# Kernel optimization log

Hardware: AMD Instinct MI355X
Metric: run time of the kernel (lower is better)

## Reference

```python
import jax, jax.numpy as jnp
import numpy as np

SEQ, D_IN, D_OUT = 4096, 1024, 1024


def setup_inputs() -> dict:
    key = jax.random.key(0)
    k_emb, k_q, k_k, k_v = jax.random.split(key, 4)
    # torch Linear stores weight as [out, in]; we keep [in, out] for x @ W
    scale = 1.0 / np.sqrt(D_IN)
    return {
        "embeddings": jax.random.normal(k_emb, (SEQ, D_IN), dtype=jnp.float32),
        "w_query": jax.random.uniform(k_q, (D_IN, D_OUT), dtype=jnp.float32, minval=-scale, maxval=scale),
        "w_key": jax.random.uniform(k_k, (D_IN, D_OUT), dtype=jnp.float32, minval=-scale, maxval=scale),
        "w_value": jax.random.uniform(k_v, (D_IN, D_OUT), dtype=jnp.float32, minval=-scale, maxval=scale),
    }


def reference(embeddings, w_query, w_key, w_value):
    # QKV projections (bias=False)
    q = embeddings @ w_query  # [S, D_out]
    k = embeddings @ w_key    # [S, D_out]
    v = embeddings @ w_value  # [S, D_out]
    inv_sqrt_d = 1.0 / jnp.sqrt(jnp.asarray(k.shape[-1], dtype=q.dtype))
    scores = jnp.einsum("sd,td->st", q, k) * inv_sqrt_d  # [S, S]
    weights = jax.nn.softmax(scores, axis=-1)
    return weights @ v  # [S, D_out]
```

## Files before the change

kernel.cpp:

```cpp
#include <hip/hip_runtime.h>
#include <hip/hip_bf16.h>

typedef unsigned short u16;
typedef __bf16 bf16x8 __attribute__((ext_vector_type(8)));
typedef float f32x4 __attribute__((ext_vector_type(4)));
typedef unsigned short u16x8 __attribute__((ext_vector_type(8)));
typedef unsigned short u16x4 __attribute__((ext_vector_type(4)));

__device__ __forceinline__ float bf2f(u16 u) {
  unsigned x = ((unsigned)u) << 16;
  return __builtin_bit_cast(float, x);
}
__device__ __forceinline__ u16 f2bf(float f) {
  unsigned u = __builtin_bit_cast(unsigned, f);
  u += 0x7fffu + ((u >> 16) & 1u);
  return (u16)(u >> 16);
}

__device__ __forceinline__ void gload16(const u16* g, u16* lds) {
  __builtin_amdgcn_global_load_lds(
      (const __attribute__((address_space(1))) void*)g,
      (__attribute__((address_space(3))) void*)lds,
      16, 0, 0);
}

__device__ __forceinline__ void bar() {
  asm volatile("" ::: "memory");
  __builtin_amdgcn_s_barrier();
  asm volatile("" ::: "memory");
}
template <int N> __device__ __forceinline__ void wait_vm() {
  asm volatile("s_waitcnt vmcnt(%0)" :: "n"(N) : "memory");
}
__device__ __forceinline__ void wait_lgkm0() {
  asm volatile("s_waitcnt lgkmcnt(0)" ::: "memory");
}

#define OFF_A(d,h) (((d)*2+(h))*8192)
#define OFF_B(d,h) (32768 + ((d)*2+(h))*8192)

struct G256 {
  const u16 *gA0, *gA1, *gB0, *gB1;
  int dst0, dst1;
  int aoff0[4], aoff1[4], boff[4];
  u16* lds;
};

__device__ __forceinline__ int swz_slot(int row, int q) {
  return row * 4 + (q ^ ((row ^ (row >> 2)) & 3));
}

__device__ __forceinline__ void mfma_quad(f32x4 (*accr)[4], const bf16x8* af, const bf16x8* bf) {
#pragma unroll
  for (int i = 0; i < 4; ++i)
#pragma unroll
    for (int j = 0; j < 4; ++j)
      accr[i][j] = __builtin_amdgcn_mfma_f32_16x16x32_bf16(af[i], bf[j], accr[i][j], 0, 0, 0);
}

template <int W3, bool S01, bool S23>
__device__ __forceinline__ void ktile256(const G256& g, int s, f32x4 (&acc)[8][4]) {
  const int d = s & 1;
  bf16x8 af[4], bf[4];
  const int kA1 = (s + 1) * 64 + 32;
  const int kA0 = (s + 2) * 64;

#pragma unroll
  for (int i = 0; i < 4; ++i) af[i] = *(const bf16x8*)(g.lds + OFF_A(d, 0) + g.aoff0[i]);
#pragma unroll
  for (int j = 0; j < 4; ++j) bf[j] = *(const bf16x8*)(g.lds + OFF_B(d, 0) + g.boff[j]);
  if (S01) {
    gload16(g.gA0 + kA1, g.lds + OFF_A(d ^ 1, 1) + g.dst0);
    gload16(g.gA1 + kA1, g.lds + OFF_A(d ^ 1, 1) + g.dst1);
    gload16(g.gB0 + kA1, g.lds + OFF_B(d ^ 1, 1) + g.dst0);
    gload16(g.gB1 + kA1, g.lds + OFF_B(d ^ 1, 1) + g.dst1);
  }
  wait_lgkm0();
  __builtin_amdgcn_s_setprio(1);
  mfma_quad(&acc[0], af, bf);
  __builtin_amdgcn_s_setprio(0);

#pragma unroll
  for (int i = 0; i < 4; ++i) af[i] = *(const bf16x8*)(g.lds + OFF_A(d, 0) + g.aoff1[i]);
  wait_lgkm0();
  bar();
  __builtin_amdgcn_s_setprio(1);
  mfma_quad(&acc[4], af, bf);
  __builtin_amdgcn_s_setprio(0);

#pragma unroll
  for (int i = 0; i < 4; ++i) af[i] = *(const bf16x8*)(g.lds + OFF_A(d, 1) + g.aoff0[i]);
#pragma unroll
  for (int j = 0; j < 4; ++j) bf[j] = *(const bf16x8*)(g.lds + OFF_B(d, 1) + g.boff[j]);
  if (S23) {
    gload16(g.gA0 + kA0, g.lds + OFF_A(d, 0) + g.dst0);
    gload16(g.gA1 + kA0, g.lds + OFF_A(d, 0) + g.dst1);
    gload16(g.gB0 + kA0, g.lds + OFF_B(d, 0) + g.dst0);
    gload16(g.gB1 + kA0, g.lds + OFF_B(d, 0) + g.dst1);
  }
  wait_lgkm0();
  __builtin_amdgcn_s_setprio(1);
  mfma_quad(&acc[0], af, bf);
  __builtin_amdgcn_s_setprio(0);

#pragma unroll
  for (int i = 0; i < 4; ++i) af[i] = *(const bf16x8*)(g.lds + OFF_A(d, 1) + g.aoff1[i]);
  wait_lgkm0();
  if constexpr (W3 >= 0) wait_vm<(W3 >= 0 ? W3 : 0)>();
  bar();
  __builtin_amdgcn_s_setprio(1);
  mfma_quad(&acc[4], af, bf);
  __builtin_amdgcn_s_setprio(0);
}

template <int OUT_MODE, int NX, int NT>
__device__ __forceinline__ void gemm256_body(
    const u16* __restrict__ A, int lda, const u16* __restrict__ B, int ldb,
    void* __restrict__ C, int ldc, float cscale, u16* lds, int bid)
{
  static_assert(NT >= 3, "tail peel needs NT>=3");
  const int by = (bid & 7) + 8 * (bid / (8 * NX));
  const int bx = (bid >> 3) % NX;
  const int m0 = by * 256, n0 = bx * 256;
  const int t = threadIdx.x;
  const int w = t >> 6, l = t & 63;
  const int wm = (w >> 2) * 128, wn = (w & 3) * 64;
  const int fr = l & 15, q = l >> 4;

  G256 g;
  g.lds = lds;
  {
    const int s0 = w * 64 + l;
    const int r0 = s0 >> 2, r1 = r0 + 128;
    const int q0 = (s0 & 3) ^ ((r0 ^ (r0 >> 2)) & 3);
    const int q1 = (s0 & 3) ^ ((r1 ^ (r1 >> 2)) & 3);
    g.gA0 = A + (size_t)(m0 + r0) * lda + q0 * 8;
    g.gA1 = A + (size_t)(m0 + r1) * lda + q1 * 8;
    g.gB0 = B + (size_t)(n0 + r0) * ldb + q0 * 8;
    g.gB1 = B + (size_t)(n0 + r1) * ldb + q1 * 8;
    g.dst0 = (w * 64) * 8;
    g.dst1 = (512 + w * 64) * 8;
  }
#pragma unroll
  for (int i = 0; i < 4; ++i) {
    g.aoff0[i] = swz_slot(wm + 16 * i + fr, q) * 8;
    g.aoff1[i] = swz_slot(wm + 64 + 16 * i + fr, q) * 8;
    g.boff[i]  = swz_slot(wn + 16 * i + fr, q) * 8;
  }

  f32x4 acc[8][4] = {};

  gload16(g.gA0 + 0,  lds + OFF_A(0, 0) + g.dst0);
  gload16(g.gA1 + 0,  lds + OFF_A(0, 0) + g.dst1);
  gload16(g.gB0 + 0,  lds + OFF_B(0, 0) + g.dst0);
  gload16(g.gB1 + 0,  lds + OFF_B(0, 0) + g.dst1);
  gload16(g.gA0 + 32, lds + OFF_A(0, 1) + g.dst0);
  gload16(g.gA1 + 32, lds + OFF_A(0, 1) + g.dst1);
  gload16(g.gB0 + 32, lds + OFF_B(0, 1) + g.dst0);
  gload16(g.gB1 + 32, lds + OFF_B(0, 1) + g.dst1);
  gload16(g.gA0 + 64, lds + OFF_A(1, 0) + g.dst0);
  gload16(g.gA1 + 64, lds + OFF_A(1, 0) + g.dst1);
  gload16(g.gB0 + 64, lds + OFF_B(1, 0) + g.dst0);
  gload16(g.gB1 + 64, lds + OFF_B(1, 0) + g.dst1);
  wait_vm<4>();
  bar();

  for (int s = 0; s + 2 < NT; ++s)
    ktile256<4, true, true>(g, s, acc);
  ktile256<0, true, false>(g, NT - 2, acc);
  ktile256<-1, false, false>(g, NT - 1, acc);

  bar();
  const int er = q * 4, ec = fr;
  const int rg = l >> 3, c = l & 7;

  if (OUT_MODE == 1) {
    u16* Ch = (u16*)C;
    u16* eb = lds + w * 4608;
#pragma unroll
    for (int half = 0; half < 2; ++half) {
#pragma unroll
      for (int i = 0; i < 4; ++i)
#pragma unroll
        for (int j = 0; j < 4; ++j)
#pragma unroll
          for (int r = 0; r < 4; ++r)
            eb[(16 * i + er + r) * 72 + 16 * j + ec] = f2bf(acc[4 * half + i][j][r] * cscale);
#pragma unroll
      for (int k = 0; k < 8; ++k) {
        const int row = k * 8 + rg;
        u16x8 v = *(const u16x8*)(eb + row * 72 + c * 8);
        *(u16x8*)(Ch + (size_t)(m0 + wm + 64 * half + row) * ldc + n0 + wn + c * 8) = v;
      }
    }
  } else {
    float* Cf = (float*)C;
    float* eb = (float*)lds + w * 2304;
#pragma unroll
    for (int half = 0; half < 2; ++half)
#pragma unroll
      for (int ip = 0; ip < 2; ++ip) {
#pragma unroll
        for (int ii = 0; ii < 2; ++ii)
#pragma unroll
          for (int j = 0; j < 4; ++j)
#pragma unroll
            for (int r = 0; r < 4; ++r)
              eb[(16 * ii + er + r) * 72 + 16 * j + ec] = acc[4 * half + 2 * ip + ii][j][r] * cscale;
#pragma unroll
        for (int k = 0; k < 4; ++k) {
          const int row = k * 8 + rg;
          float4 v0 = *(const float4*)(eb + row * 72 + c * 4);
          float4 v1 = *(const float4*)(eb + row * 72 + (c + 8) * 4);
          float* dst = Cf + (size_t)(m0 + wm + 64 * half + 32 * ip + row) * ldc + n0 + wn;
          *(float4*)(dst + c * 4) = v0;
          *(float4*)(dst + (c + 8) * 4) = v1;
        }
      }
  }
}

__global__ __launch_bounds__(512, 2) void gemm_qkv256(const u16* __restrict__ A,
                                                      const u16* __restrict__ B,
                                                      u16* __restrict__ C) {
  __shared__ __align__(16) u16 lds[65536];
  gemm256_body<1, 12, 16>(A, 1024, B, 1024, C, 3072, 1.0f, lds, blockIdx.x);
}

__global__ __launch_bounds__(512, 2) void gemm_score256(const u16* __restrict__ QKV,
                                                        u16* __restrict__ S) {
  __shared__ __align__(16) u16 lds[65536];
  gemm256_body<1, 16, 16>(QKV, 3072, QKV + 1024, 3072, S, 4096, 0.03125f, lds, blockIdx.x);
}

__global__ __launch_bounds__(512, 2) void gemm_pv256f(const u16* __restrict__ S,
                                                      const u16* __restrict__ Vt,
                                                      float* __restrict__ P4) {
  __shared__ __align__(16) u16 lds[65536];
  const int b = blockIdx.x;
  const int sp = b >> 6;
  float* Cp = P4 + (size_t)sp * 4096 * 1024;
  gemm256_body<0, 4, 16>(S + sp * 1024, 4096, Vt + sp * 1024, 4096,
                         Cp, 1024, 1.0f, lds, b & 63);
}

__global__ __launch_bounds__(512, 2) void gemm_pv256h(const u16* __restrict__ S,
                                                      const u16* __restrict__ Vt,
                                                      u16* __restrict__ P4) {
  __shared__ __align__(16) u16 lds[65536];
  const int b = blockIdx.x;
  const int sp = b >> 6;
  u16* Cp = P4 + (size_t)sp * 4096 * 1024;
  gemm256_body<1, 4, 16>(S + sp * 1024, 4096, Vt + sp * 1024, 4096,
                         Cp, 1024, 1.0f, lds, b & 63);
}

__global__ __launch_bounds__(256) void reduce4f(const float* __restrict__ P4,
                                                float* __restrict__ O) {
  const size_t i = ((size_t)blockIdx.x * 256 + threadIdx.x) * 4;
  const size_t st = (size_t)4096 * 1024;
  float4 a = *(const float4*)(P4 + i);
  float4 b = *(const float4*)(P4 + st + i);
  float4 c = *(const float4*)(P4 + 2 * st + i);
  float4 d = *(const float4*)(P4 + 3 * st + i);
  float4 o;
  o.x = (a.x + b.x) + (c.x + d.x);
  o.y = (a.y + b.y) + (c.y + d.y);
  o.z = (a.z + b.z) + (c.z + d.z);
  o.w = (a.w + b.w) + (c.w + d.w);
  *(float4*)(O + i) = o;
}

__global__ __launch_bounds__(256) void reduce4h(const u16* __restrict__ P4,
                                                float* __restrict__ O) {
  const size_t i = ((size_t)blockIdx.x * 256 + threadIdx.x) * 4;
  const size_t st = (size_t)4096 * 1024;
  u16x4 a = *(const u16x4*)(P4 + i);
  u16x4 b = *(const u16x4*)(P4 + st + i);
  u16x4 c = *(const u16x4*)(P4 + 2 * st + i);
  u16x4 d = *(const u16x4*)(P4 + 3 * st + i);
  float4 o;
  o.x = (bf2f(a.x) + bf2f(b.x)) + (bf2f(c.x) + bf2f(d.x));
  o.y = (bf2f(a.y) + bf2f(b.y)) + (bf2f(c.y) + bf2f(d.y));
  o.z = (bf2f(a.z) + bf2f(b.z)) + (bf2f(c.z) + bf2f(d.z));
  o.w = (bf2f(a.w) + bf2f(b.w)) + (bf2f(c.w) + bf2f(d.w));
  *(float4*)(O + i) = o;
}

__global__ __launch_bounds__(256) void prep(
    const float* __restrict__ E,
    const float* __restrict__ w0, const float* __restrict__ w1,
    const float* __restrict__ w2,
    u16* __restrict__ Ebf, u16* __restrict__ Wt)
{
  int b = blockIdx.x;
  if (b < 4096) {
    const int i = (b * 256 + threadIdx.x) * 4;
    float4 f = *(const float4*)(E + i);
    u16x4 o;
    o.x = f2bf(f.x); o.y = f2bf(f.y); o.z = f2bf(f.z); o.w = f2bf(f.w);
    *(u16x4*)(Ebf + i) = o;
  } else {
    b -= 4096;
    const int which = b >> 10;
    const int tile = b & 1023;
    const float* in = (which == 0) ? w0 : (which == 1) ? w1 : w2;
    u16* o = Wt + (size_t)which * 1024 * 1024;
    const int c0 = (tile & 31) * 32, r0 = (tile >> 5) * 32;
    __shared__ u16 tl[32][33];
    const int tx = threadIdx.x & 31, ty0 = threadIdx.x >> 5;
#pragma unroll
    for (int k = 0; k < 4; ++k) {
      const int ty = ty0 + k * 8;
      tl[ty][tx] = f2bf(in[(size_t)(r0 + ty) * 1024 + c0 + tx]);
    }
    __syncthreads();
#pragma unroll
    for (int k = 0; k < 4; ++k) {
      const int ty = ty0 + k * 8;
      o[(size_t)(c0 + ty) * 1024 + r0 + tx] = tl[tx][ty];
    }
  }
}

__global__ __launch_bounds__(256) void softmax_tv(u16* __restrict__ S,
                                                  const u16* __restrict__ QKV,
                                                  u16* __restrict__ Vt) {
  __shared__ float red[8];
  __shared__ u16 tl[32][33];
  const int b = blockIdx.x;
  if (b < 4096) {
    const int N = 4096;
    u16* p = S + (size_t)b * N;
    const int t = threadIdx.x;
    u16x8 u0 = ((const u16x8*)p)[t * 2];
    u16x8 u1 = ((const u16x8*)p)[t * 2 + 1];
    float v[16];
#pragma unroll
    for (int i = 0; i < 8; ++i) v[i] = bf2f(u0[i]);
#pragma unroll
    for (int i = 0; i < 8; ++i) v[8 + i] = bf2f(u1[i]);

    float m = -1e30f;
#pragma unroll
    for (int i = 0; i < 16; ++i) m = fmaxf(m, v[i]);
#pragma unroll
    for (int off = 32; off; off >>= 1) m = fmaxf(m, __shfl_xor(m, off));
    if ((t & 63) == 0) red[t >> 6] = m;
    __syncthreads();
    m = fmaxf(fmaxf(red[0], red[1]), fmaxf(red[2], red[3]));

    float s = 0.f;
#pragma unroll
    for (int i = 0; i < 16; ++i) { v[i] = __expf(v[i] - m); s += v[i]; }
#pragma unroll
    for (int off = 32; off; off >>= 1) s += __shfl_xor(s, off);
    if ((t & 63) == 0) red[4 + (t >> 6)] = s;
    __syncthreads();
    s = (red[4] + red[5]) + (red[6] + red[7]);
    const float inv = 1.0f / s;

    u16x8 o0, o1;
#pragma unroll
    for (int i = 0; i < 8; ++i) o0[i] = f2bf(v[i] * inv);
#pragma unroll
    for (int i = 0; i < 8; ++i) o1[i] = f2bf(v[8 + i] * inv);
    ((u16x8*)p)[t * 2] = o0;
    ((u16x8*)p)[t * 2 + 1] = o1;
  } else {
    const int v = b - 4096;
    const int c0 = (v & 31) * 32;
    const int r0 = (v >> 5) * 32;
    const int tx = threadIdx.x & 31, ty0 = threadIdx.x >> 5;
    const u16* Vin = QKV + 2048;
#pragma unroll
    for (int k = 0; k < 4; ++k) {
      const int ty = ty0 + k * 8;
      tl[ty][tx] = Vin[(size_t)(r0 + ty) * 3072 + c0 + tx];
    }
    __syncthreads();
#pragma unroll
    for (int k = 0; k < 4; ++k) {
      const int ty = ty0 + k * 8;
      Vt[(size_t)(c0 + ty) * 4096 + r0 + tx] = tl[tx][ty];
    }
  }
}

extern "C" void kernel_launch(void* const* d_in, const int* in_sizes, int n_in,
                              void* d_out, int out_size, void* d_ws, size_t ws_size,
                              hipStream_t stream) {
  const float* E  = (const float*)d_in[0];
  const float* Wq = (const float*)d_in[1];
  const float* Wk = (const float*)d_in[2];
  const float* Wv = (const float*)d_in[3];
  float* Out = (float*)d_out;

  char* w = (char*)d_ws;
  u16* Ebf = (u16*)(w);
  u16* Wt  = (u16*)(w + (size_t)(8u << 20));
  u16* QKV = (u16*)(w + (size_t)(14u << 20));
  u16* Vt  = (u16*)(w + (size_t)(38u << 20));
  u16* S   = (u16*)(w + (size_t)(46u << 20));

  prep<<<7168, 256, 0, stream>>>(E, Wq, Wk, Wv, Ebf, Wt);

  gemm_qkv256<<<192, 512, 0, stream>>>(Ebf, Wt, QKV);

  gemm_score256<<<256, 512, 0, stream>>>(QKV, S);

  softmax_tv<<<8192, 256, 0, stream>>>(S, QKV, Vt);

  if (ws_size >= ((size_t)146u << 20)) {
    float* P4 = (float*)(w + ((size_t)78u << 20));
    gemm_pv256f<<<256, 512, 0, stream>>>(S, Vt, P4);
    reduce4f<<<4096, 256, 0, stream>>>(P4, Out);
  } else {
    u16* P4 = (u16*)w;
    gemm_pv256h<<<256, 512, 0, stream>>>(S, Vt, P4);
    reduce4h<<<4096, 256, 0, stream>>>(P4, Out);
  }
}
```

Measured before the change: 208.6 us.

## Restructure GEMM k-loop prefetch to one barrier per tile with full-tile loads

The 256x256 GEMM main loop now uses a single barrier per k-tile instead of two. All eight global-to-LDS loads for tile s+2 are issued right after that barrier, replacing the earlier scheme that staggered half-tile loads across the k-tile. The goal is to cut barrier and wait overhead in the hot loop. The trade-off is that each tile now waits for all outstanding loads to finish (wait_vm<0>), so memory latency is hidden behind only one k-tile of MFMA work, which may expose load latency.

```diff
diff --git a/kernel.cpp b/kernel.cpp
--- a/kernel.cpp
+++ b/kernel.cpp
@@ -58,32 +58,22 @@
       accr[i][j] = __builtin_amdgcn_mfma_f32_16x16x32_bf16(af[i], bf[j], accr[i][j], 0, 0, 0);
 }
 
-template <int W3, bool S01, bool S23>
+template <bool STG>
 __device__ __forceinline__ void ktile256(const G256& g, int s, f32x4 (&acc)[8][4]) {
   const int d = s & 1;
   bf16x8 af[4], bf[4];
-  const int kA1 = (s + 1) * 64 + 32;
-  const int kA0 = (s + 2) * 64;
+  const int kt2 = (s + 2) * 64;
 
 #pragma unroll
   for (int i = 0; i < 4; ++i) af[i] = *(const bf16x8*)(g.lds + OFF_A(d, 0) + g.aoff0[i]);
 #pragma unroll
   for (int j = 0; j < 4; ++j) bf[j] = *(const bf16x8*)(g.lds + OFF_B(d, 0) + g.boff[j]);
-  if (S01) {
-    gload16(g.gA0 + kA1, g.lds + OFF_A(d ^ 1, 1) + g.dst0);
-    gload16(g.gA1 + kA1, g.lds + OFF_A(d ^ 1, 1) + g.dst1);
-    gload16(g.gB0 + kA1, g.lds + OFF_B(d ^ 1, 1) + g.dst0);
-    gload16(g.gB1 + kA1, g.lds + OFF_B(d ^ 1, 1) + g.dst1);
-  }
-  wait_lgkm0();
   __builtin_amdgcn_s_setprio(1);
   mfma_quad(&acc[0], af, bf);
   __builtin_amdgcn_s_setprio(0);
 
 #pragma unroll
   for (int i = 0; i < 4; ++i) af[i] = *(const bf16x8*)(g.lds + OFF_A(d, 0) + g.aoff1[i]);
-  wait_lgkm0();
-  bar();
   __builtin_amdgcn_s_setprio(1);
   mfma_quad(&acc[4], af, bf);
   __builtin_amdgcn_s_setprio(0);
@@ -92,13 +82,6 @@
   for (int i = 0; i < 4; ++i) af[i] = *(const bf16x8*)(g.lds + OFF_A(d, 1) + g.aoff0[i]);
 #pragma unroll
   for (int j = 0; j < 4; ++j) bf[j] = *(const bf16x8*)(g.lds + OFF_B(d, 1) + g.boff[j]);
-  if (S23) {
-    gload16(g.gA0 + kA0, g.lds + OFF_A(d, 0) + g.dst0);
-    gload16(g.gA1 + kA0, g.lds + OFF_A(d, 0) + g.dst1);
-    gload16(g.gB0 + kA0, g.lds + OFF_B(d, 0) + g.dst0);
-    gload16(g.gB1 + kA0, g.lds + OFF_B(d, 0) + g.dst1);
-  }
-  wait_lgkm0();
   __builtin_amdgcn_s_setprio(1);
   mfma_quad(&acc[0], af, bf);
   __builtin_amdgcn_s_setprio(0);
@@ -106,8 +89,18 @@
 #pragma unroll
   for (int i = 0; i < 4; ++i) af[i] = *(const bf16x8*)(g.lds + OFF_A(d, 1) + g.aoff1[i]);
   wait_lgkm0();
-  if constexpr (W3 >= 0) wait_vm<(W3 >= 0 ? W3 : 0)>();
+  wait_vm<0>();
   bar();
+  if (STG) {
+    gload16(g.gA0 + kt2,      g.lds + OFF_A(d, 0) + g.dst0);
+    gload16(g.gA1 + kt2,      g.lds + OFF_A(d, 0) + g.dst1);
+    gload16(g.gA0 + kt2 + 32, g.lds + OFF_A(d, 1) + g.dst0);
+    gload16(g.gA1 + kt2 + 32, g.lds + OFF_A(d, 1) + g.dst1);
+    gload16(g.gB0 + kt2,      g.lds + OFF_B(d, 0) + g.dst0);
+    gload16(g.gB1 + kt2,      g.lds + OFF_B(d, 0) + g.dst1);
+    gload16(g.gB0 + kt2 + 32, g.lds + OFF_B(d, 1) + g.dst0);
+    gload16(g.gB1 + kt2 + 32, g.lds + OFF_B(d, 1) + g.dst1);
+  }
   __builtin_amdgcn_s_setprio(1);
   mfma_quad(&acc[4], af, bf);
   __builtin_amdgcn_s_setprio(0);
@@ -150,25 +143,25 @@
 
   f32x4 acc[8][4] = {};
 
-  gload16(g.gA0 + 0,  lds + OFF_A(0, 0) + g.dst0);
-  gload16(g.gA1 + 0,  lds + OFF_A(0, 0) + g.dst1);
-  gload16(g.gB0 + 0,  lds + OFF_B(0, 0) + g.dst0);
-  gload16(g.gB1 + 0,  lds + OFF_B(0, 0) + g.dst1);
-  gload16(g.gA0 + 32, lds + OFF_A(0, 1) + g.dst0);
-  gload16(g.gA1 + 32, lds + OFF_A(0, 1) + g.dst1);
-  gload16(g.gB0 + 32, lds + OFF_B(0, 1) + g.dst0);
-  gload16(g.gB1 + 32, lds + OFF_B(0, 1) + g.dst1);
-  gload16(g.gA0 + 64, lds + OFF_A(1, 0) + g.dst0);
-  gload16(g.gA1 + 64, lds + OFF_A(1, 0) + g.dst1);
-  gload16(g.gB0 + 64, lds + OFF_B(1, 0) + g.dst0);
-  gload16(g.gB1 + 64, lds + OFF_B(1, 0) + g.dst1);
-  wait_vm<4>();
+#pragma unroll
+  for (int s = 0; s < 2; ++s) {
+    const int kt = s * 64, d = s & 1;
+    gload16(g.gA0 + kt,      lds + OFF_A(d, 0) + g.dst0);
+    gload16(g.gA1 + kt,      lds + OFF_A(d, 0) + g.dst1);
+    gload16(g.gA0 + kt + 32, lds + OFF_A(d, 1) + g.dst0);
+    gload16(g.gA1 + kt + 32, lds + OFF_A(d, 1) + g.dst1);
+    gload16(g.gB0 + kt,      lds + OFF_B(d, 0) + g.dst0);
+    gload16(g.gB1 + kt,      lds + OFF_B(d, 0) + g.dst1);
+    gload16(g.gB0 + kt + 32, lds + OFF_B(d, 1) + g.dst0);
+    gload16(g.gB1 + kt + 32, lds + OFF_B(d, 1) + g.dst1);
+  }
+  wait_vm<8>();
   bar();
 
   for (int s = 0; s + 2 < NT; ++s)
-    ktile256<4, true, true>(g, s, acc);
-  ktile256<0, true, false>(g, NT - 2, acc);
-  ktile256<-1, false, false>(g, NT - 1, acc);
+    ktile256<true>(g, s, acc);
+  ktile256<false>(g, NT - 2, acc);
+  ktile256<false>(g, NT - 1, acc);
 
   bar();
   const int er = q * 4, ec = fr;
```

New measurement: 213.3 us. 2.2% more time.
